# Kernel optimization log

Measured on AMD Instinct MI355X. Metric: run time of the kernel, lower is better.

Reference implementation:

```python
import jax, jax.numpy as jnp
import numpy as np

BS, N, F, G, H, L, HFC, C, E = 8, 15135, 64, 73, 256, 3, 512, 2, 242160

def setup_inputs() -> dict:
    key = jax.random.key(0)
    ks = jax.random.split(key, 16)
    s = 0.02
    return {
        "x": jax.random.normal(ks[0], (BS, N, F), jnp.float32),
        "batch": jnp.zeros((BS,), jnp.int64),
        "edge_index": jax.random.randint(ks[1], (2, E), 0, N, jnp.int64),
        "nodes_graphlets": jax.random.uniform(ks[2], (N, G), jnp.float32),
        "W1": jax.random.normal(ks[3], (F + G, H), jnp.float32) * s,
        "b1": jnp.zeros((H,), jnp.float32),
        "W2": jax.random.normal(ks[4], (H, H), jnp.float32) * s,
        "b2": jnp.zeros((H,), jnp.float32),
        "W3": jax.random.normal(ks[5], (H, H), jnp.float32) * s,
        "b3": jnp.zeros((H,), jnp.float32),
        "fc_W": jax.random.normal(ks[6], (L * H, 1), jnp.float32) * s,
        "fc_b": jnp.zeros((1,), jnp.float32),
        "lin1_W": jax.random.normal(ks[7], (N, HFC), jnp.float32) * s,
        "lin1_b": jnp.zeros((HFC,), jnp.float32),
        "lin2_W": jax.random.normal(ks[8], (HFC, C), jnp.float32) * s,
        "lin2_b": jnp.zeros((C,), jnp.float32),
    }


def reference(x, batch, edge_index, nodes_graphlets, W1, b1, W2, b2, W3, b3,
              fc_W, fc_b, lin1_W, lin1_b, lin2_W, lin2_b):
    bs, n, _ = x.shape
    row, col = edge_index[0], edge_index[1]
    # GCN normalization with self-loops (edge_weight = 1): D^-1/2 (A+I) D^-1/2
    deg = jnp.zeros((n,), x.dtype).at[col].add(1.0) + 1.0
    dis = jax.lax.rsqrt(deg)
    norm = dis[row] * dis[col]          # [E]
    deg_inv = 1.0 / deg                 # self-loop coefficient dis[i]^2

    def gcn_conv(h, W, b):
        hw = h @ W                                  # [bs, n, H]
        msg = hw[:, row, :] * norm[None, :, None]   # gather src, scale
        agg = jnp.zeros_like(hw).at[:, col, :].add(msg)
        agg = agg + hw * deg_inv[None, :, None]     # self loops
        return agg + b

    # graphlet_mode == 'input': concat graphlet features to node features
    pe = jnp.broadcast_to(nodes_graphlets[None], (bs,) + nodes_graphlets.shape)
    h = jnp.concatenate([x, pe], axis=2)            # [bs, n, F+G]

    h1 = jax.nn.elu(gcn_conv(h, W1, b1))
    h2 = jax.nn.elu(gcn_conv(h1, W2, b2))
    h3 = jax.nn.elu(gcn_conv(h2, W3, b3))

    # mode == 'cat': stack along new last dim then flatten (torch stack+view order)
    hc = jnp.stack([h1, h2, h3], axis=-1).reshape(bs, n, -1)  # [bs, n, H*L]
    g = (hc @ fc_W + fc_b).reshape(bs, n)                     # [bs, n_genes]

    z = jax.nn.elu(g @ lin1_W + lin1_b)   # dropout: eval mode -> identity
    out = z @ lin2_W + lin2_b
    return jax.nn.log_softmax(out, axis=-1)
```

## Files before the change

kernel.cpp:

```cpp
#include <hip/hip_runtime.h>
#include <hip/hip_bf16.h>

using bf16 = __hip_bfloat16;
typedef short s16x8 __attribute__((ext_vector_type(8)));
typedef short s16x4 __attribute__((ext_vector_type(4)));
typedef float f32x4 __attribute__((ext_vector_type(4)));
typedef float f32x2 __attribute__((ext_vector_type(2)));

#define BSZ   8
#define NN    15135
#define FF    64
#define GG    73
#define HH    256
#define EE    242160
#define K1P   160
#define MREAL (BSZ * NN)
#define MPAD  (946 * 128)
#define HFC   512
#define NCHUNK 64
#define NCHUNKS ((NN + NCHUNK - 1) / NCHUNK)
#define SCANB  ((NN + 255) / 256)
#define FP8_INV_SCALE 0.015625f

#define GLOAD_LDS16(gp, lp)                                                     \
    __builtin_amdgcn_global_load_lds(                                           \
        (const __attribute__((address_space(1))) void*)(gp),                    \
        (__attribute__((address_space(3))) void*)(lp), 16, 0, 0)

__device__ __forceinline__ int colmap(int p) {
    return (p & 192) | ((p & 3) << 4) | ((p >> 2) & 15);
}

#define PREP_H0_CNT (MREAL * (K1P / 8))
#define PREP_W1_CNT (256 * K1P)
#define PREP_W23_CNT 65536
#define PREP_TOT (PREP_H0_CNT + PREP_W1_CNT + 2 * PREP_W23_CNT + NN + MREAL + 64)
__global__ void k_prep(const float* __restrict__ x, const float* __restrict__ gl,
                       bf16* __restrict__ h0,
                       const float* __restrict__ W1, const float* __restrict__ W2,
                       const float* __restrict__ W3, bf16* __restrict__ W1T,
                       bf16* __restrict__ W2T, bf16* __restrict__ W3T,
                       int* __restrict__ cnt, float* __restrict__ g,
                       int* __restrict__ sync) {
    int idx = blockIdx.x * blockDim.x + threadIdx.x;
    if (idx < PREP_H0_CNT) {
        int m = idx / (K1P / 8);
        int q = idx - m * (K1P / 8);
        int j0 = q * 8;
        int n = m % NN;
        s16x8 o;
        #pragma unroll
        for (int k = 0; k < 8; ++k) {
            int j = j0 + k;
            float val;
            if (j < FF) val = x[(size_t)m * FF + j];
            else if (j < FF + GG) val = gl[(size_t)n * GG + (j - FF)];
            else val = 0.f;
            o[k] = (short)__bfloat16_as_ushort(__float2bfloat16(val));
        }
        *(s16x8*)&h0[(size_t)m * K1P + j0] = o;
        return;
    }
    idx -= PREP_H0_CNT;
    if (idx < PREP_W1_CNT) {
        int nn = idx / K1P, kk = idx - nn * K1P;
        W1T[idx] = __float2bfloat16(
            kk < FF + GG ? 64.f * W1[(size_t)kk * 256 + nn] : 0.f);
        return;
    }
    idx -= PREP_W1_CNT;
    if (idx < PREP_W23_CNT) {
        int nn = idx >> 8, kk = idx & 255;
        W2T[idx] = __float2bfloat16(64.f * W2[(size_t)colmap(kk) * 256 + nn]);
        return;
    }
    idx -= PREP_W23_CNT;
    if (idx < PREP_W23_CNT) {
        int nn = idx >> 8, kk = idx & 255;
        W3T[idx] = __float2bfloat16(64.f * W3[(size_t)colmap(kk) * 256 + nn]);
        return;
    }
    idx -= PREP_W23_CNT;
    if (idx < NN) { cnt[idx] = 0; return; }
    idx -= NN;
    if (idx < MREAL) { g[idx] = 0.f; return; }
    idx -= MREAL;
    if (idx < 64) sync[idx] = 0;
}

#define NB_SETUP 240
#define TS 1024
__device__ __forceinline__ void gbar(int* sync, int target) {
    __syncthreads();
    if (threadIdx.x == 0) {
        __threadfence();
        atomicAdd(sync, 1);
        while (__hip_atomic_load(sync, __ATOMIC_RELAXED,
                                 __HIP_MEMORY_SCOPE_AGENT) < target)
            __builtin_amdgcn_s_sleep(2);
        __threadfence();
    }
    __syncthreads();
}

__global__ __launch_bounds__(1024)
void k_setup(const int* __restrict__ erow, const int* __restrict__ ecol,
             int* __restrict__ cnt, int* __restrict__ offs,
             int* __restrict__ cursor, int* __restrict__ bsum,
             float* __restrict__ dis, float* __restrict__ dinv,
             int2* __restrict__ cpack, int* __restrict__ sync) {
    __shared__ int ws2[16];
    __shared__ int carry;
    const int tid = threadIdx.x, bid = blockIdx.x;
    const int gid = bid * TS + tid;

    if (gid < EE) atomicAdd(&cnt[ecol[gid]], 1);
    gbar(sync, NB_SETUP);

    if (bid == 0) {
        if (tid == 0) carry = 0;
        __syncthreads();
        for (int base = 0; base < NN; base += TS) {
            int i = base + tid;
            int v = (i < NN) ? cnt[i] : 0;
            int lane = tid & 63, w = tid >> 6;
            int s = v;
            #pragma unroll
            for (int off = 1; off < 64; off <<= 1) {
                int t = __shfl_up(s, off);
                if (lane >= off) s += t;
            }
            if (lane == 63) ws2[w] = s;
            __syncthreads();
            int pre = 0;
            #pragma unroll
            for (int k = 0; k < 16; ++k) pre += (k < w) ? ws2[k] : 0;
            int incl = carry + pre + s;
            int excl = incl - v;
            if (i < NN) {
                offs[i]   = excl;
                cursor[i] = excl;
                float d = (float)(v + 1);
                dis[i]  = rsqrtf(d);
                dinv[i] = (1.0f / d) * FP8_INV_SCALE;
            }
            __syncthreads();
            if (tid == TS - 1) carry = incl;
            __syncthreads();
        }
        if (tid == 0) offs[NN] = carry;
    }
    gbar(sync, 2 * NB_SETUP);

    if (gid < EE) {
        int r = erow[gid], c = ecol[gid];
        int p = atomicAdd(&cursor[c], 1);
        cpack[p] = make_int2(r, __float_as_int(dis[r] * dis[c] * FP8_INV_SCALE));
    }
}

#define BK 32
template <int K>
__global__ __launch_bounds__(256)
void k_gemm(const bf16* __restrict__ A, const bf16* __restrict__ BT,
            unsigned char* __restrict__ C) {
    __shared__ __align__(16) short As[64 * BK];
    __shared__ __align__(16) short Bs[256 * BK];
    const int tid  = threadIdx.x;
    const int bm   = blockIdx.x * 64;
    const int lane = tid & 63, wave = tid >> 6;
    const int wn   = wave * 64;
    const int fr   = lane & 15, quad = lane >> 4;
    const int r    = tid >> 2;
    const int c    = (tid & 3) * 8;

    const bf16* Ap = A  + (size_t)(bm + r) * K + c;
    const bf16* Bp = BT + (size_t)r * K + c;
    short* AsT = As + tid * 8;
    short* BsT = Bs + tid * 8;

    f32x4 acc[4][4] = {};

    for (int k0 = 0; k0 < K; k0 += BK) {
        GLOAD_LDS16(Ap + k0, AsT);
        #pragma unroll
        for (int q = 0; q < 4; ++q)
            GLOAD_LDS16(Bp + (size_t)(q * 64) * K + k0, BsT + q * 64 * BK);
        __syncthreads();
        s16x8 af[4], bfv[4];
        #pragma unroll
        for (int i = 0; i < 4; ++i)
            af[i] = *(const s16x8*)&As[(i * 16 + fr) * BK + quad * 8];
        #pragma unroll
        for (int j = 0; j < 4; ++j)
            bfv[j] = *(const s16x8*)&Bs[(wn + j * 16 + fr) * BK + quad * 8];
        #pragma unroll
        for (int i = 0; i < 4; ++i)
            #pragma unroll
            for (int j = 0; j < 4; ++j)
                acc[i][j] = __builtin_amdgcn_mfma_f32_16x16x32_bf16(
                    af[i], bfv[j], acc[i][j], 0, 0, 0);
        __syncthreads();
    }

    #pragma unroll
    for (int i = 0; i < 4; ++i) {
        int rbase = bm + i * 16 + quad * 4;
        #pragma unroll
        for (int rr = 0; rr < 4; ++rr) {
            int row = rbase + rr;
            if (row >= MREAL) continue;
            unsigned wpack = (unsigned)__builtin_amdgcn_cvt_pk_fp8_f32(
                acc[i][0][rr], acc[i][1][rr], 0, false);
            wpack = (unsigned)__builtin_amdgcn_cvt_pk_fp8_f32(
                acc[i][2][rr], acc[i][3][rr], (int)wpack, true);
            *(unsigned*)&C[(size_t)row * 256 + wn + fr * 4] = wpack;
        }
    }
}

#define AGG_GRP 512
#define AGG_STRIDE (AGG_GRP * 4)
__global__ __launch_bounds__(256)
void k_agg(const unsigned char* __restrict__ hw, bf16* __restrict__ hout,
           const int* __restrict__ offs, const int2* __restrict__ cpack,
           const float* __restrict__ dinv,
           const float* __restrict__ bias, const float* __restrict__ fcW,
           float* __restrict__ g, int writeH) {
    const int b    = blockIdx.x & 7;
    const int grp  = blockIdx.x >> 3;
    const int wid  = threadIdx.x >> 6;
    const int lane = threadIdx.x & 63;
    const int wv   = grp * 4 + wid;
    const unsigned c4 = lane * 4;

    const unsigned char* hwb = hw + (size_t)b * NN * 256;

    float bias4[4], fw4[4];
    #pragma unroll
    for (int k = 0; k < 4; ++k) {
        int cl = colmap((int)c4 + k);
        bias4[k] = bias[cl];
        fw4[k]   = fcW[3 * cl];
    }

    for (int v0 = wv; v0 < NN; v0 += AGG_STRIDE) {
        const int v   = __builtin_amdgcn_readfirstlane(v0);
        const int beg = __builtin_amdgcn_readfirstlane(offs[v]);
        const int end = __builtin_amdgcn_readfirstlane(offs[v + 1]);
        const float di = dinv[v];
        f32x2 a01, a23;
        {
            unsigned q = *(const unsigned*)(hwb + (((unsigned)v) << 8) + c4);
            f32x2 t0 = __builtin_amdgcn_cvt_pk_f32_fp8(q, false);
            f32x2 t1 = __builtin_amdgcn_cvt_pk_f32_fp8(q, true);
            f32x2 dd = {di, di};
            a01 = dd * t0;
            a23 = dd * t1;
        }

        #define EDGE1(qv, mv) {                                            \
            f32x2 t0 = __builtin_amdgcn_cvt_pk_f32_fp8((qv), false);       \
            f32x2 t1 = __builtin_amdgcn_cvt_pk_f32_fp8((qv), true);        \
            f32x2 mm = {(mv), (mv)};                                       \
            a01 += mm * t0;                                                \
            a23 += mm * t1; }

        int e = beg;
        while (e + 16 <= end) {
            int2 ep[16];
            #pragma unroll
            for (int u = 0; u < 16; ++u) ep[u] = cpack[e + u];
            unsigned q[16];
            #pragma unroll
            for (int u = 0; u < 16; ++u)
                q[u] = *(const unsigned*)(hwb + (((unsigned)ep[u].x) << 8) + c4);
            #pragma unroll
            for (int u = 0; u < 16; ++u) EDGE1(q[u], __int_as_float(ep[u].y));
            e += 16;
        }
        if (e + 8 <= end) {
            int2 ep[8];
            #pragma unroll
            for (int u = 0; u < 8; ++u) ep[u] = cpack[e + u];
            unsigned q[8];
            #pragma unroll
            for (int u = 0; u < 8; ++u)
                q[u] = *(const unsigned*)(hwb + (((unsigned)ep[u].x) << 8) + c4);
            #pragma unroll
            for (int u = 0; u < 8; ++u) EDGE1(q[u], __int_as_float(ep[u].y));
            e += 8;
        }
        if (e + 4 <= end) {
            int2 ep[4];
            #pragma unroll
            for (int u = 0; u < 4; ++u) ep[u] = cpack[e + u];
            unsigned q[4];
            #pragma unroll
            for (int u = 0; u < 4; ++u)
                q[u] = *(const unsigned*)(hwb + (((unsigned)ep[u].x) << 8) + c4);
            #pragma unroll
            for (int u = 0; u < 4; ++u) EDGE1(q[u], __int_as_float(ep[u].y));
            e += 4;
        }
        if (e + 2 <= end) {
            int2 ep0 = cpack[e], ep1 = cpack[e + 1];
            unsigned q0 = *(const unsigned*)(hwb + (((unsigned)ep0.x) << 8) + c4);
            unsigned q1 = *(const unsigned*)(hwb + (((unsigned)ep1.x) << 8) + c4);
            EDGE1(q0, __int_as_float(ep0.y));
            EDGE1(q1, __int_as_float(ep1.y));
            e += 2;
        }
        if (e < end) {
            int2 ep0 = cpack[e];
            unsigned q0 = *(const unsigned*)(hwb + (((unsigned)ep0.x) << 8) + c4);
            EDGE1(q0, __int_as_float(ep0.y));
        }
        #undef EDGE1

        float acc4[4] = {a01[0], a01[1], a23[0], a23[1]};
        float p = 0.f;
        s16x4 o4;
        #pragma unroll
        for (int k = 0; k < 4; ++k) {
            float hv = acc4[k] + bias4[k];
            hv = hv > 0.f ? hv : (__expf(hv) - 1.0f);
            o4[k] = (short)__bfloat16_as_ushort(__float2bfloat16(hv));
            p += hv * fw4[k];
        }
        if (writeH)
            *(s16x4*)&hout[((size_t)b * NN + v) * 256 + c4] = o4;

        #pragma unroll
        for (int off = 32; off; off >>= 1) p += __shfl_xor(p, off);
        if (lane == 0) g[(size_t)b * NN + v] += p;
    }
}

__global__ __launch_bounds__(256)
void k_lin1(const float* __restrict__ g, const float* __restrict__ fcb,
            const float* __restrict__ W, float* __restrict__ zpart) {
    const int ny = blockIdx.x;
    const int n0 = ny * NCHUNK;
    const int cnt = min(NCHUNK, NN - n0);
    const int tid = threadIdx.x;
    __shared__ float sg[8][NCHUNK];
    float fb = fcb[0];
    for (int idx = tid; idx < 8 * NCHUNK; idx += 256) {
        int b = idx / NCHUNK, nn = idx - b * NCHUNK;
        sg[b][nn] = (nn < cnt) ? (g[(size_t)b * NN + n0 + nn] + fb) : 0.f;
    }
    __syncthreads();
    float2 acc[8] = {};
    for (int nn = 0; nn < cnt; ++nn) {
        float2 w = *(const float2*)&W[(size_t)(n0 + nn) * HFC + tid * 2];
        #pragma unroll
        for (int b = 0; b < 8; ++b) {
            float gv = sg[b][nn];
            acc[b].x += gv * w.x;
            acc[b].y += gv * w.y;
        }
    }
    #pragma unroll
    for (int b = 0; b < 8; ++b)
        *(float2*)&zpart[(size_t)ny * 4096 + b * 512 + tid * 2] = acc[b];
}

__global__ __launch_bounds__(512)
void k_lin2(const float* __restrict__ zpart, const float* __restrict__ l1b,
            const float* __restrict__ W2, const float* __restrict__ l2b,
            float* __restrict__ out) {
    __shared__ float r0[512], r1[512];
    const int b = blockIdx.x, t = threadIdx.x;
    float s = 0.f;
    for (int c = 0; c < NCHUNKS; ++c) s += zpart[(size_t)c * 4096 + b * 512 + t];
    float zv = s + l1b[t];
    zv = zv > 0.f ? zv : (__expf(zv) - 1.0f);
    r0[t] = zv * W2[t * 2 + 0];
    r1[t] = zv * W2[t * 2 + 1];
    __syncthreads();
    for (int st = 256; st; st >>= 1) {
        if (t < st) { r0[t] += r0[t + st]; r1[t] += r1[t + st]; }
        __syncthreads();
    }
    if (t == 0) {
        float o0 = r0[0] + l2b[0], o1 = r1[0] + l2b[1];
        float m = fmaxf(o0, o1);
        float lse = m + logf(expf(o0 - m) + expf(o1 - m));
        out[b * 2 + 0] = o0 - lse;
        out[b * 2 + 1] = o1 - lse;
    }
}

extern "C" void kernel_launch(void* const* d_in, const int* in_sizes, int n_in,
                              void* d_out, int out_size, void* d_ws, size_t ws_size,
                              hipStream_t stream) {
    const float* x    = (const float*)d_in[0];
    const int*   eidx = (const int*)d_in[2];
    const float* gl   = (const float*)d_in[3];
    const float* W1   = (const float*)d_in[4];
    const float* b1   = (const float*)d_in[5];
    const float* W2   = (const float*)d_in[6];
    const float* b2   = (const float*)d_in[7];
    const float* W3   = (const float*)d_in[8];
    const float* b3   = (const float*)d_in[9];
    const float* fcW  = (const float*)d_in[10];
    const float* fcb  = (const float*)d_in[11];
    const float* l1W  = (const float*)d_in[12];
    const float* l1b  = (const float*)d_in[13];
    const float* l2W  = (const float*)d_in[14];
    const float* l2b  = (const float*)d_in[15];
    float* out = (float*)d_out;

    size_t off = 0;
    auto alloc = [&](size_t bytes) {
        void* p = (char*)d_ws + off;
        off += (bytes + 255) & ~(size_t)255;
        return p;
    };
    bf16* bufA          = (bf16*)alloc((size_t)MPAD * 256 * 2);
    unsigned char* bufC = (unsigned char*)alloc((size_t)MPAD * 256);
    bf16* W1T      = (bf16*)alloc(256 * K1P * 2);
    bf16* W2T      = (bf16*)alloc(256 * 256 * 2);
    bf16* W3T      = (bf16*)alloc(256 * 256 * 2);
    int*  deg_cnt  = (int*)alloc(NN * 4);
    int*  offs     = (int*)alloc((NN + 1) * 4);
    int*  cursor   = (int*)alloc(NN * 4);
    int*  bsum     = (int*)alloc(SCANB * 4);
    float* dis     = (float*)alloc(NN * 4);
    float* dinv    = (float*)alloc(NN * 4);
    int2* cpack    = (int2*)alloc((size_t)EE * 8);
    float* g       = (float*)alloc((size_t)BSZ * NN * 4);
    int*  sync     = (int*)alloc(64 * 4);

    float* zpart = (float*)bufC;

    const int* erow = eidx;
    const int* ecol = eidx + EE;

    k_prep<<<(PREP_TOT + 255) / 256, 256, 0, stream>>>(
        x, gl, bufA, W1, W2, W3, W1T, W2T, W3T, deg_cnt, g, sync);

    k_setup<<<NB_SETUP, TS, 0, stream>>>(erow, ecol, deg_cnt, offs, cursor,
                                         bsum, dis, dinv, cpack, sync);

    dim3 ggrid(MPAD / 64);
    dim3 agrid(8 * AGG_GRP);

    k_gemm<K1P><<<ggrid, 256, 0, stream>>>(bufA, W1T, bufC);
    k_agg<<<agrid, 256, 0, stream>>>(bufC, bufA, offs, cpack, dinv,
                                     b1, fcW + 0, g, 1);
    k_gemm<256><<<ggrid, 256, 0, stream>>>(bufA, W2T, bufC);
    k_agg<<<agrid, 256, 0, stream>>>(bufC, bufA, offs, cpack, dinv,
                                     b2, fcW + 1, g, 1);
    k_gemm<256><<<ggrid, 256, 0, stream>>>(bufA, W3T, bufC);
    k_agg<<<agrid, 256, 0, stream>>>(bufC, bufA, offs, cpack, dinv,
                                     b3, fcW + 2, g, 0);

    k_lin1<<<NCHUNKS, 256, 0, stream>>>(g, fcb, l1W, zpart);
    k_lin2<<<8, 512, 0, stream>>>(zpart, l1b, l2W, l2b, out);
}
```

Baseline: 457.7 us.

## Replace serial single-block scan and second grid barrier with per-block LDS scan

Each setup block now redundantly computes the full degree prefix scan in shared memory, which removes the serial scan in block 0 and the second grid-wide barrier. The remaining barrier uses hierarchical counters spread over eight groups to reduce contention on one atomic. Normalisation factors are computed from the scanned offsets instead of stored dis/dinv arrays, and the aggregation kernel derives the self-loop coefficient from the edge range. The cost is about 60KB of LDS per block and redundant scan work in all 240 blocks, and the hierarchical barrier assumes exactly 30 blocks per group.

```diff
diff --git a/kernel.cpp b/kernel.cpp
--- a/kernel.cpp
+++ b/kernel.cpp
@@ -19,7 +19,6 @@
 #define HFC   512
 #define NCHUNK 64
 #define NCHUNKS ((NN + NCHUNK - 1) / NCHUNK)
-#define SCANB  ((NN + 255) / 256)
 #define FP8_INV_SCALE 0.015625f
 
 #define GLOAD_LDS16(gp, lp)                                                     \
@@ -34,14 +33,14 @@
 #define PREP_H0_CNT (MREAL * (K1P / 8))
 #define PREP_W1_CNT (256 * K1P)
 #define PREP_W23_CNT 65536
-#define PREP_TOT (PREP_H0_CNT + PREP_W1_CNT + 2 * PREP_W23_CNT + NN + MREAL + 64)
+#define PREP_TOT (PREP_H0_CNT + PREP_W1_CNT + 2 * PREP_W23_CNT + 2 * NN + MREAL + 1024)
 __global__ void k_prep(const float* __restrict__ x, const float* __restrict__ gl,
                        bf16* __restrict__ h0,
                        const float* __restrict__ W1, const float* __restrict__ W2,
                        const float* __restrict__ W3, bf16* __restrict__ W1T,
                        bf16* __restrict__ W2T, bf16* __restrict__ W3T,
-                       int* __restrict__ cnt, float* __restrict__ g,
-                       int* __restrict__ sync) {
+                       int* __restrict__ cnt, int* __restrict__ cnt2,
+                       float* __restrict__ g, int* __restrict__ sync) {
     int idx = blockIdx.x * blockDim.x + threadIdx.x;
     if (idx < PREP_H0_CNT) {
         int m = idx / (K1P / 8);
@@ -83,20 +82,24 @@
     idx -= PREP_W23_CNT;
     if (idx < NN) { cnt[idx] = 0; return; }
     idx -= NN;
+    if (idx < NN) { cnt2[idx] = 0; return; }
+    idx -= NN;
     if (idx < MREAL) { g[idx] = 0.f; return; }
     idx -= MREAL;
-    if (idx < 64) sync[idx] = 0;
+    if (idx < 1024) sync[idx] = 0;
 }
 
 #define NB_SETUP 240
 #define TS 1024
-__device__ __forceinline__ void gbar(int* sync, int target) {
+__device__ __forceinline__ void gbar_once(int* sync) {
     __syncthreads();
     if (threadIdx.x == 0) {
         __threadfence();
-        atomicAdd(sync, 1);
-        while (__hip_atomic_load(sync, __ATOMIC_RELAXED,
-                                 __HIP_MEMORY_SCOPE_AGENT) < target)
+        int grp = blockIdx.x & 7;
+        int old = atomicAdd(&sync[16 * (grp + 1)], 1);
+        if (old == 29) atomicAdd(&sync[0], 1);
+        while (__hip_atomic_load(&sync[0], __ATOMIC_RELAXED,
+                                 __HIP_MEMORY_SCOPE_AGENT) < 8)
             __builtin_amdgcn_s_sleep(2);
         __threadfence();
     }
@@ -106,56 +109,78 @@
 __global__ __launch_bounds__(1024)
 void k_setup(const int* __restrict__ erow, const int* __restrict__ ecol,
              int* __restrict__ cnt, int* __restrict__ offs,
-             int* __restrict__ cursor, int* __restrict__ bsum,
-             float* __restrict__ dis, float* __restrict__ dinv,
-             int2* __restrict__ cpack, int* __restrict__ sync) {
-    __shared__ int ws2[16];
-    __shared__ int carry;
+             int* __restrict__ cnt2, int2* __restrict__ cpack,
+             int* __restrict__ sync) {
+    __shared__ int soffs[NN + 1];
+    __shared__ int wtot[16], wpre[16];
     const int tid = threadIdx.x, bid = blockIdx.x;
     const int gid = bid * TS + tid;
-
-    if (gid < EE) atomicAdd(&cnt[ecol[gid]], 1);
-    gbar(sync, NB_SETUP);
-
-    if (bid == 0) {
-        if (tid == 0) carry = 0;
-        __syncthreads();
-        for (int base = 0; base < NN; base += TS) {
-            int i = base + tid;
-            int v = (i < NN) ? cnt[i] : 0;
-            int lane = tid & 63, w = tid >> 6;
+    const int lane = tid & 63, w = tid >> 6;
+
+    int myc = 0, myr = 0;
+    if (gid < EE) {
+        myc = ecol[gid];
+        myr = erow[gid];
+        atomicAdd(&cnt[myc], 1);
+    }
+    gbar_once(sync);
+
+    {
+        const int base = w * 946;
+        int carry = 0;
+        #pragma unroll
+        for (int j = 0; j < 15; ++j) {
+            int o = j * 64 + lane;
+            int i = base + o;
+            bool in = o < 946;
+            int v = (in && i < NN) ? cnt[i] : 0;
             int s = v;
             #pragma unroll
             for (int off = 1; off < 64; off <<= 1) {
                 int t = __shfl_up(s, off);
                 if (lane >= off) s += t;
             }
-            if (lane == 63) ws2[w] = s;
-            __syncthreads();
-            int pre = 0;
-            #pragma unroll
-            for (int k = 0; k < 16; ++k) pre += (k < w) ? ws2[k] : 0;
-            int incl = carry + pre + s;
-            int excl = incl - v;
-            if (i < NN) {
-                offs[i]   = excl;
-                cursor[i] = excl;
-                float d = (float)(v + 1);
-                dis[i]  = rsqrtf(d);
-                dinv[i] = (1.0f / d) * FP8_INV_SCALE;
+            if (in) soffs[i] = carry + s - v;
+            carry += __shfl(s, 63);
+        }
+        if (lane == 0) wtot[w] = carry;
+    }
+    __syncthreads();
+    if (w == 0 && lane < 16) {
+        int t = wtot[lane];
+        int s = t;
+        #pragma unroll
+        for (int off = 1; off < 16; off <<= 1) {
+            int u = __shfl_up(s, off);
+            if (lane >= off) s += u;
+        }
+        wpre[lane] = s - t;
+    }
+    __syncthreads();
+    {
+        const int base = w * 946;
+        int add = wpre[w];
+        if (add) {
+            #pragma unroll
+            for (int j = 0; j < 15; ++j) {
+                int o = j * 64 + lane;
+                if (o < 946) soffs[base + o] += add;
             }
-            __syncthreads();
-            if (tid == TS - 1) carry = incl;
-            __syncthreads();
-        }
-        if (tid == 0) offs[NN] = carry;
-    }
-    gbar(sync, 2 * NB_SETUP);
+        }
+    }
+    __syncthreads();
+
+    if (bid == 0)
+        for (int i = tid; i <= NN; i += TS) offs[i] = soffs[i];
 
     if (gid < EE) {
-        int r = erow[gid], c = ecol[gid];
-        int p = atomicAdd(&cursor[c], 1);
-        cpack[p] = make_int2(r, __float_as_int(dis[r] * dis[c] * FP8_INV_SCALE));
+        int bc = soffs[myc], dc = soffs[myc + 1] - bc;
+        int br = soffs[myr], dr = soffs[myr + 1] - br;
+        (void)br;
+        int p = atomicAdd(&cnt2[myc], 1);
+        float norm = rsqrtf((float)(dr + 1)) * rsqrtf((float)(dc + 1))
+                     * FP8_INV_SCALE;
+        cpack[bc + p] = make_int2(myr, __float_as_int(norm));
     }
 }
 
@@ -224,7 +249,6 @@
 __global__ __launch_bounds__(256)
 void k_agg(const unsigned char* __restrict__ hw, bf16* __restrict__ hout,
            const int* __restrict__ offs, const int2* __restrict__ cpack,
-           const float* __restrict__ dinv,
            const float* __restrict__ bias, const float* __restrict__ fcW,
            float* __restrict__ g, int writeH) {
     const int b    = blockIdx.x & 7;
@@ -248,7 +272,7 @@
         const int v   = __builtin_amdgcn_readfirstlane(v0);
         const int beg = __builtin_amdgcn_readfirstlane(offs[v]);
         const int end = __builtin_amdgcn_readfirstlane(offs[v + 1]);
-        const float di = dinv[v];
+        const float di = FP8_INV_SCALE / (float)(end - beg + 1);
         f32x2 a01, a23;
         {
             unsigned q = *(const unsigned*)(hwb + (((unsigned)v) << 8) + c4);
@@ -425,13 +449,10 @@
     bf16* W3T      = (bf16*)alloc(256 * 256 * 2);
     int*  deg_cnt  = (int*)alloc(NN * 4);
     int*  offs     = (int*)alloc((NN + 1) * 4);
-    int*  cursor   = (int*)alloc(NN * 4);
-    int*  bsum     = (int*)alloc(SCANB * 4);
-    float* dis     = (float*)alloc(NN * 4);
-    float* dinv    = (float*)alloc(NN * 4);
+    int*  cnt2     = (int*)alloc(NN * 4);
     int2* cpack    = (int2*)alloc((size_t)EE * 8);
     float* g       = (float*)alloc((size_t)BSZ * NN * 4);
-    int*  sync     = (int*)alloc(64 * 4);
+    int*  sync     = (int*)alloc(1024 * 4);
 
     float* zpart = (float*)bufC;
 
@@ -439,22 +460,22 @@
     const int* ecol = eidx + EE;
 
     k_prep<<<(PREP_TOT + 255) / 256, 256, 0, stream>>>(
-        x, gl, bufA, W1, W2, W3, W1T, W2T, W3T, deg_cnt, g, sync);
-
-    k_setup<<<NB_SETUP, TS, 0, stream>>>(erow, ecol, deg_cnt, offs, cursor,
-                                         bsum, dis, dinv, cpack, sync);
+        x, gl, bufA, W1, W2, W3, W1T, W2T, W3T, deg_cnt, cnt2, g, sync);
+
+    k_setup<<<NB_SETUP, TS, 0, stream>>>(erow, ecol, deg_cnt, offs, cnt2,
+                                         cpack, sync);
 
     dim3 ggrid(MPAD / 64);
     dim3 agrid(8 * AGG_GRP);
 
     k_gemm<K1P><<<ggrid, 256, 0, stream>>>(bufA, W1T, bufC);
-    k_agg<<<agrid, 256, 0, stream>>>(bufC, bufA, offs, cpack, dinv,
+    k_agg<<<agrid, 256, 0, stream>>>(bufC, bufA, offs, cpack,
                                      b1, fcW + 0, g, 1);
     k_gemm<256><<<ggrid, 256, 0, stream>>>(bufA, W2T, bufC);
-    k_agg<<<agrid, 256, 0, stream>>>(bufC, bufA, offs, cpack, dinv,
+    k_agg<<<agrid, 256, 0, stream>>>(bufC, bufA, offs, cpack,
                                      b2, fcW + 1, g, 1);
     k_gemm<256><<<ggrid, 256, 0, stream>>>(bufA, W3T, bufC);
-    k_agg<<<agrid, 256, 0, stream>>>(bufC, bufA, offs, cpack, dinv,
+    k_agg<<<agrid, 256, 0, stream>>>(bufC, bufA, offs, cpack,
                                      b3, fcW + 2, g, 0);
 
     k_lin1<<<NCHUNKS, 256, 0, stream>>>(g, fcb, l1W, zpart);
```

After: 439.1 us. -4.1%, faster.
